# Kernel tuning notes

Measured on AMD Instinct MI355X. Metric: run time of the kernel, lower is better.

Reference implementation:

```python
import jax, jax.numpy as jnp
import numpy as np


def setup_inputs() -> dict:
    key = jax.random.key(0)
    k1, k2 = jax.random.split(key)
    set1 = jax.random.normal(k1, (8, 4096, 3), dtype=jnp.float32)
    set2 = jax.random.normal(k2, (8, 4096, 3), dtype=jnp.float32)
    return {"set1": set1, "set2": set2}


def reference(set1, set2):
    # set1: [b, n, d], set2: [b, m, d]
    n = set1.shape[1]
    x2 = jnp.sum(set1 * set1, axis=-1)            # [b, n]
    y2 = jnp.sum(set2 * set2, axis=-1)            # [b, m]
    xy = jnp.einsum('bnd,bmd->bnm', set1, set2)   # [b, n, m]
    d2 = x2[:, :, None] + y2[:, None, :] - 2.0 * xy
    dist = jnp.sqrt(jnp.maximum(d2, 0.0))         # torch.cdist(p=2)
    out_dist = jnp.min(dist, axis=2)              # [b, n]
    out_dist2 = jnp.min(dist, axis=1)             # [b, m]
    total = jnp.mean(out_dist) + jnp.mean(out_dist2)
    return total / n
```

## Files before the change

### kernel.cpp

```cpp
#include <hip/hip_runtime.h>
#include <math.h>
#include <float.h>


#define NPTS 4096

typedef __attribute__((ext_vector_type(8)))  _Float16 f16x8;
typedef __attribute__((ext_vector_type(16))) float    f32x16;

static __device__ __forceinline__ unsigned h2u(_Float16 h) {
    return (unsigned)__builtin_bit_cast(unsigned short, h);
}
static __device__ __forceinline__ unsigned pack2(unsigned a, unsigned b) {
    return (a & 0xFFFFu) | (b << 16);
}

__device__ __forceinline__ float fold16(const f32x16 c, float m) {
    m = fminf(fminf(c[0],  c[1]),  m);
    m = fminf(fminf(c[2],  c[3]),  m);
    m = fminf(fminf(c[4],  c[5]),  m);
    m = fminf(fminf(c[6],  c[7]),  m);
    m = fminf(fminf(c[8],  c[9]),  m);
    m = fminf(fminf(c[10], c[11]), m);
    m = fminf(fminf(c[12], c[13]), m);
    m = fminf(fminf(c[14], c[15]), m);
    return m;
}

__global__ __launch_bounds__(512, 4)
void chamfer_fused(const float* __restrict__ set1,
                   const float* __restrict__ set2,
                   float* __restrict__ out)
{
    __shared__ uint4 frag[NPTS];

    const int blk = blockIdx.x;
    const int dir = blk >> 8;
    const int rem = blk & 255;
    const int b   = rem >> 5;
    const int qc  = rem & 31;

    const float* __restrict__ Q  = (dir ? set2 : set1) + (size_t)b * NPTS * 3;
    const float* __restrict__ DB = (dir ? set1 : set2) + (size_t)b * NPTS * 3;

    const int t    = threadIdx.x;
    const int lane = t & 63;
    const int w    = t >> 6;
    const int col  = lane & 31;
    const int half = lane >> 5;
    const int qbase = qc * 128;

    #pragma unroll
    for (int k = 0; k < 8; ++k) {
        const int p = t + 512 * k;
        const float x = DB[3 * p + 0];
        const float y = DB[3 * p + 1];
        const float z = DB[3 * p + 2];
        const _Float16 hx = (_Float16)x, hy = (_Float16)y, hz = (_Float16)z;
        const _Float16 lx = (_Float16)(x - (float)hx);
        const _Float16 ly = (_Float16)(y - (float)hy);
        const _Float16 lz = (_Float16)(z - (float)hz);
        const float p2 = fmaf(x, x, fmaf(y, y, z * z));
        const _Float16 p2h = (_Float16)p2;
        const _Float16 p2l = (_Float16)(p2 - (float)p2h);
        frag[p] = make_uint4(pack2(h2u(hx),  h2u(hy)),
                             pack2(h2u(hz),  h2u(lx)),
                             pack2(h2u(ly),  h2u(lz)),
                             pack2(h2u(p2h), h2u(p2l)));
    }

    f16x8 Bf[4];
    #pragma unroll
    for (int j = 0; j < 4; ++j) {
        const float* qp = Q + (size_t)(qbase + j * 32 + col) * 3;
        const float qx = qp[0], qy = qp[1], qz = qp[2];
        const _Float16 hx = (_Float16)qx, hy = (_Float16)qy, hz = (_Float16)qz;
        uint4 bv;
        if (!half) {
            const unsigned mx = h2u((_Float16)(-2.0f * (float)hx));
            const unsigned my = h2u((_Float16)(-2.0f * (float)hy));
            const unsigned mz = h2u((_Float16)(-2.0f * (float)hz));
            const unsigned one = 0x3C00u;
            bv = make_uint4(pack2(mx, my), pack2(mz, mx),
                            pack2(my, mz), pack2(one, one));
        } else {
            const unsigned mx = h2u((_Float16)(-2.0f * (qx - (float)hx)));
            const unsigned my = h2u((_Float16)(-2.0f * (qy - (float)hy)));
            const unsigned mz = h2u((_Float16)(-2.0f * (qz - (float)hz)));
            bv = make_uint4(pack2(mx, my), pack2(mz, 0), 0u, 0u);
        }
        Bf[j] = __builtin_bit_cast(f16x8, bv);
    }

    __syncthreads();

    const unsigned mY  = half ? 0x0000FFFFu : 0xFFFFFFFFu;
    const unsigned mZW = half ? 0u          : 0xFFFFFFFFu;
    const uint4* __restrict__ fb = frag + w * 512 + col;

    const f32x16 z16 = {0,0,0,0,0,0,0,0,0,0,0,0,0,0,0,0};
    float dm0 = FLT_MAX, dm1 = FLT_MAX, dm2 = FLT_MAX, dm3 = FLT_MAX;

    uint4 u = fb[0];
    for (int pt = 0; pt < 16; ++pt) {
        uint4 un = u;
        if (pt < 15) un = fb[(pt + 1) * 32];
        const uint4 am = make_uint4(u.x, u.y & mY, u.z & mZW, u.w & mZW);
        const f16x8 av = __builtin_bit_cast(f16x8, am);
        f32x16 c0 = __builtin_amdgcn_mfma_f32_32x32x16_f16(av, Bf[0], z16, 0, 0, 0);
        f32x16 c1 = __builtin_amdgcn_mfma_f32_32x32x16_f16(av, Bf[1], z16, 0, 0, 0);
        dm0 = fold16(c0, dm0);
        c0 = __builtin_amdgcn_mfma_f32_32x32x16_f16(av, Bf[2], z16, 0, 0, 0);
        dm1 = fold16(c1, dm1);
        c1 = __builtin_amdgcn_mfma_f32_32x32x16_f16(av, Bf[3], z16, 0, 0, 0);
        dm2 = fold16(c0, dm2);
        dm3 = fold16(c1, dm3);
        u = un;
    }

    float dmin[4] = {dm0, dm1, dm2, dm3};
    __syncthreads();
    float* part = (float*)frag;
    #pragma unroll
    for (int j = 0; j < 4; ++j) {
        const float v = fminf(dmin[j], __shfl_xor(dmin[j], 32));
        if (!half) part[w * 128 + j * 32 + col] = v;
    }
    __syncthreads();

    float dist = 0.0f;
    if (t < 128) {
        float m = part[t];
        #pragma unroll
        for (int ww = 1; ww < 8; ++ww)
            m = fminf(m, part[ww * 128 + t]);
        const float* qp = Q + (size_t)(qbase + t) * 3;
        const float q2 = fmaf(qp[0], qp[0], fmaf(qp[1], qp[1], qp[2] * qp[2]));
        dist = sqrtf(fmaxf(q2 + m, 0.0f));
    }
    #pragma unroll
    for (int off = 32; off > 0; off >>= 1)
        dist += __shfl_down(dist, off);
    if (t < 128 && (t & 63) == 0)
        atomicAdd(out, dist * (1.0f / 134217728.0f));
}

extern "C" void kernel_launch(void* const* d_in, const int* in_sizes, int n_in,
                              void* d_out, int out_size, void* d_ws, size_t ws_size,
                              hipStream_t stream) {
    const float* s1 = (const float*)d_in[0];
    const float* s2 = (const float*)d_in[1];
    float* out = (float*)d_out;

    hipMemsetAsync(out, 0, sizeof(float), stream);
    chamfer_fused<<<dim3(512), dim3(512), 0, stream>>>(s1, s2, out);
}
```

Before: 73.82 us.

## Halve query tile per block and double-buffer database staging in LDS

Each block now handles 64 queries instead of 128, so the grid doubles to 1024 blocks. The database is staged through two 1024-point LDS buffers in four phases, with global loads for the next chunk issued while MFMAs process the current one. This cuts LDS use per block and overlaps load and convert latency with compute. The cost is that each database point is converted twice as often across the grid, and each phase adds a barrier.

```diff
diff --git a/kernel.cpp b/kernel.cpp
--- a/kernel.cpp
+++ b/kernel.cpp
@@ -13,6 +13,19 @@
 }
 static __device__ __forceinline__ unsigned pack2(unsigned a, unsigned b) {
     return (a & 0xFFFFu) | (b << 16);
+}
+static __device__ __forceinline__ uint4 packpt(float x, float y, float z) {
+    const _Float16 hx = (_Float16)x, hy = (_Float16)y, hz = (_Float16)z;
+    const _Float16 lx = (_Float16)(x - (float)hx);
+    const _Float16 ly = (_Float16)(y - (float)hy);
+    const _Float16 lz = (_Float16)(z - (float)hz);
+    const float p2 = fmaf(x, x, fmaf(y, y, z * z));
+    const _Float16 p2h = (_Float16)p2;
+    const _Float16 p2l = (_Float16)(p2 - (float)p2h);
+    return make_uint4(pack2(h2u(hx),  h2u(hy)),
+                      pack2(h2u(hz),  h2u(lx)),
+                      pack2(h2u(ly),  h2u(lz)),
+                      pack2(h2u(p2h), h2u(p2l)));
 }
 
 __device__ __forceinline__ float fold16(const f32x16 c, float m) {
@@ -32,13 +45,13 @@
                    const float* __restrict__ set2,
                    float* __restrict__ out)
 {
-    __shared__ uint4 frag[NPTS];
+    __shared__ uint4 buf[2][1024];
 
     const int blk = blockIdx.x;
-    const int dir = blk >> 8;
-    const int rem = blk & 255;
-    const int b   = rem >> 5;
-    const int qc  = rem & 31;
+    const int dir = blk >> 9;
+    const int rem = blk & 511;
+    const int b   = rem >> 6;
+    const int qc  = rem & 63;
 
     const float* __restrict__ Q  = (dir ? set2 : set1) + (size_t)b * NPTS * 3;
     const float* __restrict__ DB = (dir ? set1 : set2) + (size_t)b * NPTS * 3;
@@ -48,30 +61,11 @@
     const int w    = t >> 6;
     const int col  = lane & 31;
     const int half = lane >> 5;
-    const int qbase = qc * 128;
+    const int qbase = qc * 64;
 
+    f16x8 Bf0, Bf1;
     #pragma unroll
-    for (int k = 0; k < 8; ++k) {
-        const int p = t + 512 * k;
-        const float x = DB[3 * p + 0];
-        const float y = DB[3 * p + 1];
-        const float z = DB[3 * p + 2];
-        const _Float16 hx = (_Float16)x, hy = (_Float16)y, hz = (_Float16)z;
-        const _Float16 lx = (_Float16)(x - (float)hx);
-        const _Float16 ly = (_Float16)(y - (float)hy);
-        const _Float16 lz = (_Float16)(z - (float)hz);
-        const float p2 = fmaf(x, x, fmaf(y, y, z * z));
-        const _Float16 p2h = (_Float16)p2;
-        const _Float16 p2l = (_Float16)(p2 - (float)p2h);
-        frag[p] = make_uint4(pack2(h2u(hx),  h2u(hy)),
-                             pack2(h2u(hz),  h2u(lx)),
-                             pack2(h2u(ly),  h2u(lz)),
-                             pack2(h2u(p2h), h2u(p2l)));
-    }
-
-    f16x8 Bf[4];
-    #pragma unroll
-    for (int j = 0; j < 4; ++j) {
+    for (int j = 0; j < 2; ++j) {
         const float* qp = Q + (size_t)(qbase + j * 32 + col) * 3;
         const float qx = qp[0], qy = qp[1], qz = qp[2];
         const _Float16 hx = (_Float16)qx, hy = (_Float16)qy, hz = (_Float16)qz;
@@ -89,51 +83,75 @@
             const unsigned mz = h2u((_Float16)(-2.0f * (qz - (float)hz)));
             bv = make_uint4(pack2(mx, my), pack2(mz, 0), 0u, 0u);
         }
-        Bf[j] = __builtin_bit_cast(f16x8, bv);
+        if (j == 0) Bf0 = __builtin_bit_cast(f16x8, bv);
+        else        Bf1 = __builtin_bit_cast(f16x8, bv);
     }
 
+    {
+        const float* s = DB + 3 * t;
+        buf[0][t]       = packpt(s[0], s[1], s[2]);
+        const float* s2 = DB + 3 * (t + 512);
+        buf[0][t + 512] = packpt(s2[0], s2[1], s2[2]);
+    }
     __syncthreads();
 
     const unsigned mY  = half ? 0x0000FFFFu : 0xFFFFFFFFu;
     const unsigned mZW = half ? 0u          : 0xFFFFFFFFu;
-    const uint4* __restrict__ fb = frag + w * 512 + col;
+    const f32x16 z16 = {0,0,0,0,0,0,0,0,0,0,0,0,0,0,0,0};
+    float dm0 = FLT_MAX, dm1 = FLT_MAX;
 
-    const f32x16 z16 = {0,0,0,0,0,0,0,0,0,0,0,0,0,0,0,0};
-    float dm0 = FLT_MAX, dm1 = FLT_MAX, dm2 = FLT_MAX, dm3 = FLT_MAX;
+    for (int h = 0; h < 4; ++h) {
+        const uint4* __restrict__ fb = &buf[h & 1][w * 128 + col];
+        const uint4 u0 = fb[0];
+        const uint4 u1 = fb[32];
+        const uint4 u2 = fb[64];
+        const uint4 u3 = fb[96];
 
-    uint4 u = fb[0];
-    for (int pt = 0; pt < 16; ++pt) {
-        uint4 un = u;
-        if (pt < 15) un = fb[(pt + 1) * 32];
-        const uint4 am = make_uint4(u.x, u.y & mY, u.z & mZW, u.w & mZW);
-        const f16x8 av = __builtin_bit_cast(f16x8, am);
-        f32x16 c0 = __builtin_amdgcn_mfma_f32_32x32x16_f16(av, Bf[0], z16, 0, 0, 0);
-        f32x16 c1 = __builtin_amdgcn_mfma_f32_32x32x16_f16(av, Bf[1], z16, 0, 0, 0);
-        dm0 = fold16(c0, dm0);
-        c0 = __builtin_amdgcn_mfma_f32_32x32x16_f16(av, Bf[2], z16, 0, 0, 0);
-        dm1 = fold16(c1, dm1);
-        c1 = __builtin_amdgcn_mfma_f32_32x32x16_f16(av, Bf[3], z16, 0, 0, 0);
-        dm2 = fold16(c0, dm2);
-        dm3 = fold16(c1, dm3);
-        u = un;
+        float sx0 = 0, sy0 = 0, sz0 = 0, sx1 = 0, sy1 = 0, sz1 = 0;
+        if (h < 3) {
+            const float* s = DB + 3 * ((h + 1) * 1024 + t);
+            sx0 = s[0]; sy0 = s[1]; sz0 = s[2];
+            const float* s2 = s + 3 * 512;
+            sx1 = s2[0]; sy1 = s2[1]; sz1 = s2[2];
+        }
+
+        #define TILE(U) do {                                                   \
+            const uint4 am = make_uint4((U).x, (U).y & mY,                     \
+                                        (U).z & mZW, (U).w & mZW);             \
+            const f16x8 av = __builtin_bit_cast(f16x8, am);                    \
+            const f32x16 c0 =                                                  \
+                __builtin_amdgcn_mfma_f32_32x32x16_f16(av, Bf0, z16, 0, 0, 0); \
+            const f32x16 c1 =                                                  \
+                __builtin_amdgcn_mfma_f32_32x32x16_f16(av, Bf1, z16, 0, 0, 0); \
+            dm0 = fold16(c0, dm0);                                             \
+            dm1 = fold16(c1, dm1);                                             \
+        } while (0)
+
+        TILE(u0); TILE(u1); TILE(u2); TILE(u3);
+        #undef TILE
+
+        if (h < 3) {
+            buf[(h + 1) & 1][t]       = packpt(sx0, sy0, sz0);
+            buf[(h + 1) & 1][t + 512] = packpt(sx1, sy1, sz1);
+        }
+        __syncthreads();
     }
 
-    float dmin[4] = {dm0, dm1, dm2, dm3};
-    __syncthreads();
-    float* part = (float*)frag;
-    #pragma unroll
-    for (int j = 0; j < 4; ++j) {
-        const float v = fminf(dmin[j], __shfl_xor(dmin[j], 32));
-        if (!half) part[w * 128 + j * 32 + col] = v;
+    const float v0 = fminf(dm0, __shfl_xor(dm0, 32));
+    const float v1 = fminf(dm1, __shfl_xor(dm1, 32));
+    float* part = (float*)&buf[0][0];
+    if (!half) {
+        part[w * 64 + col]      = v0;
+        part[w * 64 + 32 + col] = v1;
     }
     __syncthreads();
 
     float dist = 0.0f;
-    if (t < 128) {
+    if (t < 64) {
         float m = part[t];
         #pragma unroll
         for (int ww = 1; ww < 8; ++ww)
-            m = fminf(m, part[ww * 128 + t]);
+            m = fminf(m, part[ww * 64 + t]);
         const float* qp = Q + (size_t)(qbase + t) * 3;
         const float q2 = fmaf(qp[0], qp[0], fmaf(qp[1], qp[1], qp[2] * qp[2]));
         dist = sqrtf(fmaxf(q2 + m, 0.0f));
@@ -141,7 +159,7 @@
     #pragma unroll
     for (int off = 32; off > 0; off >>= 1)
         dist += __shfl_down(dist, off);
-    if (t < 128 && (t & 63) == 0)
+    if (t == 0)
         atomicAdd(out, dist * (1.0f / 134217728.0f));
 }
 
@@ -153,5 +171,5 @@
     float* out = (float*)d_out;
 
     hipMemsetAsync(out, 0, sizeof(float), stream);
-    chamfer_fused<<<dim3(512), dim3(512), 0, stream>>>(s1, s2, out);
+    chamfer_fused<<<dim3(1024), dim3(512), 0, stream>>>(s1, s2, out);
 }
```

After: 74.18 us. Within noise of the previous version (+0.5%).
